# Performance work log

Measured on AMD Instinct MI355X. Metric: run time of the kernel, lower is better.

The kernel has to match this reference:

```python
import jax, jax.numpy as jnp
import numpy as np

N1, N2, F = 512, 512, 128
H = 512  # hidden width


def _xavier(key, shape):
    fan_in, fan_out = shape
    std = (2.0 / (fan_in + fan_out)) ** 0.5
    return jax.random.normal(key, shape, dtype=jnp.float32) * std


def setup_inputs() -> dict:
    key = jax.random.key(0)
    ks = jax.random.split(key, 8)
    V1 = jax.random.normal(ks[0], (1, N1, F), dtype=jnp.float32)
    V2 = jax.random.normal(ks[1], (1, N2, F), dtype=jnp.float32)
    W1 = _xavier(ks[2], (2 * F, H))
    b1 = 0.0001 + 5e-05 * jax.random.normal(ks[3], (H,), dtype=jnp.float32)
    W2 = _xavier(ks[4], (H, H))
    b2 = 0.0001 + 5e-05 * jax.random.normal(ks[5], (H,), dtype=jnp.float32)
    W3 = _xavier(ks[6], (H, 2))
    b3 = 0.0001 + 5e-05 * jax.random.normal(ks[7], (2,), dtype=jnp.float32)
    return {"V1": V1, "V2": V2, "W1": W1, "b1": b1, "W2": W2, "b2": b2, "W3": W3, "b3": b3}


def reference(V1, V2, W1, b1, W2, b2, W3, b3):
    n1, n2, f = V1.shape[1], V2.shape[1], V1.shape[2]
    # Fused broadcast-concat replacing the N1*N2 Python double loop
    # (i outer, j inner; V1[i] first, V2[j] second -> row-major reshape matches stack order)
    pairs = jnp.concatenate([
        jnp.broadcast_to(V1[0][:, None, :], (n1, n2, f)),
        jnp.broadcast_to(V2[0][None, :, :], (n1, n2, f)),
    ], axis=-1).reshape(1, n1 * n2, 2 * f)
    h = jax.nn.relu(pairs @ W1 + b1)
    h = jax.nn.relu(h @ W2 + b2)
    out = jax.nn.relu(h @ W3 + b3)  # final LinearEmbedding also has ReLU by default
    return out
```

## Files before the change

### kernel.cpp

```cpp
#include <hip/hip_runtime.h>


typedef short bf16x8 __attribute__((ext_vector_type(8)));
typedef float f32x16 __attribute__((ext_vector_type(16)));

#define NROW 512
#define FDIM 128
#define HDIM 512

__device__ __forceinline__ unsigned int pk2(float x, float y) {
  unsigned int r;
  asm("v_cvt_pk_bf16_f32 %0, %1, %2" : "=v"(r) : "v"(x), "v"(y));
  return r;
}

__global__ __launch_bounds__(256) void prep_ab(
    const float* __restrict__ V1, const float* __restrict__ V2,
    const float* __restrict__ W1, const float* __restrict__ b1,
    float* __restrict__ Ap, float* __restrict__ Bp) {
  __shared__ float sv[4 * FDIM];
  const int b = blockIdx.x;
  const int t = threadIdx.x;
  const bool isB = b >= 128;
  const int r0 = (b & 127) * 4;
  const float* V = isB ? V2 : V1;
  const float* W = W1 + (isB ? FDIM * HDIM : 0);
  for (int idx = t; idx < 4 * FDIM; idx += 256) sv[idx] = V[r0 * FDIM + idx];
  __syncthreads();
  float s[4][2] = {};
  for (int k = 0; k < FDIM; ++k) {
    const float w0 = W[k * HDIM + t];
    const float w1 = W[k * HDIM + t + 256];
#pragma unroll
    for (int r = 0; r < 4; ++r) {
      const float v = sv[r * FDIM + k];
      s[r][0] += v * w0;
      s[r][1] += v * w1;
    }
  }
  float* O = isB ? Bp : Ap;
  const float bb0 = isB ? 0.f : b1[t];
  const float bb1 = isB ? 0.f : b1[t + 256];
#pragma unroll
  for (int r = 0; r < 4; ++r) {
    O[(r0 + r) * HDIM + t] = s[r][0] + bb0;
    O[(r0 + r) * HDIM + t + 256] = s[r][1] + bb1;
  }
}

__global__ __launch_bounds__(256) void prep_w2(const float* __restrict__ W2,
                                               unsigned short* __restrict__ W2T) {
  const int o = blockIdx.x * 256 + threadIdx.x;
  const int kc = o >> 9;
  const int n = o & 511;
  unsigned int u[4];
#pragma unroll
  for (int e2 = 0; e2 < 4; ++e2)
    u[e2] = pk2(W2[(kc * 8 + 2 * e2) * HDIM + n], W2[(kc * 8 + 2 * e2 + 1) * HDIM + n]);
  *(uint4*)(W2T + (size_t)o * 8) = make_uint4(u[0], u[1], u[2], u[3]);
}

__global__ __launch_bounds__(512, 2) void mlp_main(
    const float* __restrict__ Ap, const float* __restrict__ Bp,
    const unsigned short* __restrict__ W2T, const float* __restrict__ b2,
    const float* __restrict__ W3, const float* __restrict__ b3,
    float* __restrict__ out) {
  extern __shared__ char smem[];
  char* sA = smem;

  const int tid = threadIdx.x;
  const int wave = tid >> 6;
  const int lane = tid & 63;
  const int cl = lane & 31;
  const int hi = lane >> 5;
  const int r15 = lane & 15;

  const int m0 = blockIdx.x * 128;
  const int i = m0 >> 9;
  const int j0 = m0 & 511;

  {
    const int c = tid & 63;
    const int rsub = tid >> 6;
    const float4 a0 = *(const float4*)(Ap + i * HDIM + c * 8);
    const float4 a1 = *(const float4*)(Ap + i * HDIM + c * 8 + 4);
#pragma unroll
    for (int it = 0; it < 16; ++it) {
      const int row = it * 8 + rsub;
      const float4 g0 = *(const float4*)(Bp + (size_t)(j0 + row) * HDIM + c * 8);
      const float4 g1 = *(const float4*)(Bp + (size_t)(j0 + row) * HDIM + c * 8 + 4);
      const uint4 v = make_uint4(
          pk2(fmaxf(a0.x + g0.x, 0.f), fmaxf(a0.y + g0.y, 0.f)),
          pk2(fmaxf(a0.z + g0.z, 0.f), fmaxf(a0.w + g0.w, 0.f)),
          pk2(fmaxf(a1.x + g1.x, 0.f), fmaxf(a1.y + g1.y, 0.f)),
          pk2(fmaxf(a1.z + g1.z, 0.f), fmaxf(a1.w + g1.w, 0.f)));
      *(uint4*)(sA + row * 1024 + ((c ^ (row & 15)) << 4)) = v;
    }
  }

  float w30[2], w31[2], bb[2];
#pragma unroll
  for (int nt = 0; nt < 2; ++nt) {
    const int n = (wave << 6) + (nt << 5) + cl;
    w30[nt] = W3[2 * n];
    w31[nt] = W3[2 * n + 1];
    bb[nt] = b2[n];
  }
  const float bb3_0 = b3[0], bb3_1 = b3[1];

  __syncthreads();

  f32x16 acc[4][2];
#pragma unroll
  for (int mt = 0; mt < 4; ++mt)
#pragma unroll
    for (int nt = 0; nt < 2; ++nt)
#pragma unroll
      for (int q = 0; q < 16; ++q) acc[mt][nt][q] = 0.f;

  const char* abase0 = sA + cl * 1024;
  const char* bbase = (const char*)W2T + (((wave << 6) + cl) << 4) + (hi << 13);

  bf16x8 af[2][4], bfr[3][2];
  {
    const int off = (hi ^ r15) << 4;
#pragma unroll
    for (int mt = 0; mt < 4; ++mt) af[0][mt] = *(const bf16x8*)(abase0 + mt * 32768 + off);
#pragma unroll
    for (int q = 0; q < 3; ++q) {
      const char* bp = bbase + ((size_t)q << 14);
      bfr[q][0] = *(const bf16x8*)(bp);
      bfr[q][1] = *(const bf16x8*)(bp + (1 << 9));
    }
  }
#pragma unroll
  for (int s = 0; s < 32; ++s) {
    const int cur = s & 1;
    if (s < 31) {
      const int off = ((((s + 1) << 1) | hi) ^ r15) << 4;
#pragma unroll
      for (int mt = 0; mt < 4; ++mt)
        af[cur ^ 1][mt] = *(const bf16x8*)(abase0 + mt * 32768 + off);
    }
    if (s < 30) {
      const char* bp = bbase + ((size_t)(s + 2) << 14);
      bfr[(s + 2) % 3][0] = *(const bf16x8*)(bp);
      bfr[(s + 2) % 3][1] = *(const bf16x8*)(bp + (1 << 9));
    }
    __builtin_amdgcn_s_setprio(1);
#pragma unroll
    for (int nt = 0; nt < 2; ++nt)
#pragma unroll
      for (int mt = 0; mt < 4; ++mt)
        acc[mt][nt] = __builtin_amdgcn_mfma_f32_32x32x16_bf16(af[cur][mt], bfr[s % 3][nt],
                                                              acc[mt][nt], 0, 0, 0);
    __builtin_amdgcn_s_setprio(0);
  }

  __syncthreads();

#pragma unroll
  for (int mt = 0; mt < 4; ++mt) {
#pragma unroll
    for (int rp = 0; rp < 8; ++rp) {
      const int ra = 2 * rp;
      const float h0a = fmaxf(acc[mt][0][ra] + bb[0], 0.f);
      const float h1a = fmaxf(acc[mt][1][ra] + bb[1], 0.f);
      const float h0b = fmaxf(acc[mt][0][ra + 1] + bb[0], 0.f);
      const float h1b = fmaxf(acc[mt][1][ra + 1] + bb[1], 0.f);
      const float4 v = make_float4(h0a * w30[0] + h1a * w30[1], h0a * w31[0] + h1a * w31[1],
                                   h0b * w30[0] + h1b * w30[1], h0b * w31[0] + h1b * w31[1]);
      const int rpi = ((ra & 3) + 8 * (ra >> 2) + 4 * hi) >> 1;
      *(float4*)(smem + rpi * 4096 + (((wave << 5) + cl) << 4)) = v;
    }
    __syncthreads();
    if (tid < 256) {
      const int rpi = tid >> 4;
      const int sub = tid & 15;
      float4 s = make_float4(0.f, 0.f, 0.f, 0.f);
#pragma unroll
      for (int k = 0; k < 16; ++k) {
        const float4 v = *(const float4*)(smem + rpi * 4096 + ((sub + (k << 4)) << 4));
        s.x += v.x; s.y += v.y; s.z += v.z; s.w += v.w;
      }
#pragma unroll
      for (int d = 1; d < 16; d <<= 1) {
        s.x += __shfl_xor(s.x, d, 64);
        s.y += __shfl_xor(s.y, d, 64);
        s.z += __shfl_xor(s.z, d, 64);
        s.w += __shfl_xor(s.w, d, 64);
      }
      if (sub == 0) {
        const int rg = m0 + (mt << 5) + (rpi << 1);
        *(float4*)(out + rg * 2) =
            make_float4(fmaxf(s.x + bb3_0, 0.f), fmaxf(s.y + bb3_1, 0.f),
                        fmaxf(s.z + bb3_0, 0.f), fmaxf(s.w + bb3_1, 0.f));
      }
    }
    __syncthreads();
  }
}

extern "C" void kernel_launch(void* const* d_in, const int* in_sizes, int n_in,
                              void* d_out, int out_size, void* d_ws, size_t ws_size,
                              hipStream_t stream) {
  const float* V1 = (const float*)d_in[0];
  const float* V2 = (const float*)d_in[1];
  const float* W1 = (const float*)d_in[2];
  const float* b1 = (const float*)d_in[3];
  const float* W2 = (const float*)d_in[4];
  const float* b2 = (const float*)d_in[5];
  const float* W3 = (const float*)d_in[6];
  const float* b3 = (const float*)d_in[7];

  float* Ap = (float*)d_ws;
  float* Bp = Ap + NROW * HDIM;
  unsigned short* W2T = (unsigned short*)(Bp + NROW * HDIM);

  const int smem_bytes = 131072;
  (void)hipFuncSetAttribute((const void*)mlp_main,
                            hipFuncAttributeMaxDynamicSharedMemorySize, smem_bytes);

  prep_ab<<<256, 256, 0, stream>>>(V1, V2, W1, b1, Ap, Bp);
  prep_w2<<<128, 256, 0, stream>>>(W2, W2T);
  mlp_main<<<2048, 512, smem_bytes, stream>>>(Ap, Bp, W2T, b2, W3, b3, (float*)d_out);
}
```

Measured before the change: 152.5 us.

## Make main kernel persistent and overlap A-tile construction with MFMA via K-half double buffering

The main kernel now launches 256 blocks, each looping over 8 row tiles, instead of one block per tile. The bf16 A tile is split into two K-halves held in double-buffered LDS. Each half for the next stage (the second half of this tile, or the first half of the next tile) is built from Ap/Bp and written while MFMAs run on the current half. This hides the global-load and convert cost of the A fill that previously ran serially before compute, and W2 fragments are prefetched across tile boundaries. In exchange, LDS grows to 160KB, the epilogue is split into smaller reduction rounds with more barriers, s_setprio hints are dropped, and the last tile prefetches one row past Ap.

```diff
diff --git a/kernel.cpp b/kernel.cpp
--- a/kernel.cpp
+++ b/kernel.cpp
@@ -60,13 +60,28 @@
   *(uint4*)(W2T + (size_t)o * 8) = make_uint4(u[0], u[1], u[2], u[3]);
 }
 
+__device__ __forceinline__ void fill_w(char* sAbuf, int w, int rsub, int c32,
+                                       const float4& a0, const float4& a1,
+                                       const float* bpn) {
+  const int row = w * 16 + rsub;
+  const float* bp = bpn + (size_t)row * HDIM;
+  const float4 g0 = *(const float4*)(bp);
+  const float4 g1 = *(const float4*)(bp + 4);
+  const uint4 v = make_uint4(
+      pk2(fmaxf(a0.x + g0.x, 0.f), fmaxf(a0.y + g0.y, 0.f)),
+      pk2(fmaxf(a0.z + g0.z, 0.f), fmaxf(a0.w + g0.w, 0.f)),
+      pk2(fmaxf(a1.x + g1.x, 0.f), fmaxf(a1.y + g1.y, 0.f)),
+      pk2(fmaxf(a1.z + g1.z, 0.f), fmaxf(a1.w + g1.w, 0.f)));
+  *(uint4*)(sAbuf + row * 512 + ((c32 ^ rsub) << 4)) = v;
+}
+
 __global__ __launch_bounds__(512, 2) void mlp_main(
     const float* __restrict__ Ap, const float* __restrict__ Bp,
     const unsigned short* __restrict__ W2T, const float* __restrict__ b2,
     const float* __restrict__ W3, const float* __restrict__ b3,
     float* __restrict__ out) {
   extern __shared__ char smem[];
-  char* sA = smem;
+  char* epi = smem + 131072;
 
   const int tid = threadIdx.x;
   const int wave = tid >> 6;
@@ -74,29 +89,9 @@
   const int cl = lane & 31;
   const int hi = lane >> 5;
   const int r15 = lane & 15;
-
-  const int m0 = blockIdx.x * 128;
-  const int i = m0 >> 9;
-  const int j0 = m0 & 511;
-
-  {
-    const int c = tid & 63;
-    const int rsub = tid >> 6;
-    const float4 a0 = *(const float4*)(Ap + i * HDIM + c * 8);
-    const float4 a1 = *(const float4*)(Ap + i * HDIM + c * 8 + 4);
-#pragma unroll
-    for (int it = 0; it < 16; ++it) {
-      const int row = it * 8 + rsub;
-      const float4 g0 = *(const float4*)(Bp + (size_t)(j0 + row) * HDIM + c * 8);
-      const float4 g1 = *(const float4*)(Bp + (size_t)(j0 + row) * HDIM + c * 8 + 4);
-      const uint4 v = make_uint4(
-          pk2(fmaxf(a0.x + g0.x, 0.f), fmaxf(a0.y + g0.y, 0.f)),
-          pk2(fmaxf(a0.z + g0.z, 0.f), fmaxf(a0.w + g0.w, 0.f)),
-          pk2(fmaxf(a1.x + g1.x, 0.f), fmaxf(a1.y + g1.y, 0.f)),
-          pk2(fmaxf(a1.z + g1.z, 0.f), fmaxf(a1.w + g1.w, 0.f)));
-      *(uint4*)(sA + row * 1024 + ((c ^ (row & 15)) << 4)) = v;
-    }
-  }
+  const int c32 = tid & 31;
+  const int rsub = tid >> 5;
+  const int bid = blockIdx.x;
 
   float w30[2], w31[2], bb[2];
 #pragma unroll
@@ -108,96 +103,136 @@
   }
   const float bb3_0 = b3[0], bb3_1 = b3[1];
 
+  const char* bbase = (const char*)W2T + (((wave << 6) + cl) << 4) + (hi << 13);
+
+  f32x16 acc[4][2];
+#pragma unroll
+  for (int mt = 0; mt < 4; ++mt)
+#pragma unroll
+    for (int nt = 0; nt < 2; ++nt)
+#pragma unroll
+      for (int q = 0; q < 16; ++q) acc[mt][nt][q] = 0.f;
+
+  bf16x8 af[2][4], bfr[4][2];
+
+#pragma unroll
+  for (int q = 0; q < 3; ++q) {
+    const char* bp = bbase + ((size_t)q << 14);
+    bfr[q][0] = *(const bf16x8*)(bp);
+    bfr[q][1] = *(const bf16x8*)(bp + (1 << 9));
+  }
+
+  {
+    const int m00 = bid * 1024;
+    const int i0 = m00 >> 9;
+    const int j00 = m00 & 511;
+    const int kh = c32 * 8;
+    const float4 a0 = *(const float4*)(Ap + i0 * HDIM + kh);
+    const float4 a1 = *(const float4*)(Ap + i0 * HDIM + kh + 4);
+    const float* bpn = Bp + (size_t)j00 * HDIM + kh;
+#pragma unroll
+    for (int w = 0; w < 8; ++w) fill_w(smem, w, rsub, c32, a0, a1, bpn);
+  }
   __syncthreads();
 
-  f32x16 acc[4][2];
-#pragma unroll
-  for (int mt = 0; mt < 4; ++mt)
-#pragma unroll
-    for (int nt = 0; nt < 2; ++nt)
-#pragma unroll
-      for (int q = 0; q < 16; ++q) acc[mt][nt][q] = 0.f;
-
-  const char* abase0 = sA + cl * 1024;
-  const char* bbase = (const char*)W2T + (((wave << 6) + cl) << 4) + (hi << 13);
-
-  bf16x8 af[2][4], bfr[3][2];
-  {
-    const int off = (hi ^ r15) << 4;
-#pragma unroll
-    for (int mt = 0; mt < 4; ++mt) af[0][mt] = *(const bf16x8*)(abase0 + mt * 32768 + off);
-#pragma unroll
-    for (int q = 0; q < 3; ++q) {
-      const char* bp = bbase + ((size_t)q << 14);
-      bfr[q][0] = *(const bf16x8*)(bp);
-      bfr[q][1] = *(const bf16x8*)(bp + (1 << 9));
+  for (int t = 0; t < 8; ++t) {
+    const int tl = bid * 8 + t;
+    const int m0 = tl * 128;
+#pragma unroll
+    for (int h = 0; h < 2; ++h) {
+      char* sAbuf = smem + h * 65536;
+      char* sAnext = smem + (h ^ 1) * 65536;
+      const int tln = (h == 0) ? tl : tl + 1;
+      const int hn = h ^ 1;
+      const int m0n = tln * 128;
+      const int in_ = m0n >> 9;
+      const int j0n = m0n & 511;
+      const int khn = hn * 256 + c32 * 8;
+      const float4 a0n = *(const float4*)(Ap + (size_t)in_ * HDIM + khn);
+      const float4 a1n = *(const float4*)(Ap + (size_t)in_ * HDIM + khn + 4);
+      const float* bpn = Bp + (size_t)j0n * HDIM + khn;
+
+      const char* alane = sAbuf + cl * 512;
+      {
+        const int off = (hi ^ r15) << 4;
+#pragma unroll
+        for (int mt = 0; mt < 4; ++mt)
+          af[0][mt] = *(const bf16x8*)(alane + mt * 16384 + off);
+      }
+#pragma unroll
+      for (int s = 0; s < 16; ++s) {
+        const int sg = h * 16 + s;
+        {
+          const int pg = (sg + 3) & 31;
+          const char* bp = bbase + ((size_t)pg << 14);
+          bfr[pg & 3][0] = *(const bf16x8*)(bp);
+          bfr[pg & 3][1] = *(const bf16x8*)(bp + (1 << 9));
+        }
+        if (s < 15) {
+          const int off = ((((s + 1) << 1) | hi) ^ r15) << 4;
+#pragma unroll
+          for (int mt = 0; mt < 4; ++mt)
+            af[(s + 1) & 1][mt] = *(const bf16x8*)(alane + mt * 16384 + off);
+        }
+        if (s & 1) fill_w(sAnext, s >> 1, rsub, c32, a0n, a1n, bpn);
+#pragma unroll
+        for (int nt = 0; nt < 2; ++nt)
+#pragma unroll
+          for (int mt = 0; mt < 4; ++mt)
+            acc[mt][nt] = __builtin_amdgcn_mfma_f32_32x32x16_bf16(
+                af[s & 1][mt], bfr[sg & 3][nt], acc[mt][nt], 0, 0, 0);
+      }
+      __syncthreads();
     }
-  }
-#pragma unroll
-  for (int s = 0; s < 32; ++s) {
-    const int cur = s & 1;
-    if (s < 31) {
-      const int off = ((((s + 1) << 1) | hi) ^ r15) << 4;
-#pragma unroll
-      for (int mt = 0; mt < 4; ++mt)
-        af[cur ^ 1][mt] = *(const bf16x8*)(abase0 + mt * 32768 + off);
+
+#pragma unroll
+    for (int mt = 0; mt < 4; ++mt) {
+#pragma unroll
+      for (int g = 0; g < 2; ++g) {
+#pragma unroll
+        for (int rr = 0; rr < 4; ++rr) {
+          const int ra = 8 * g + 2 * rr;
+          const float h0a = fmaxf(acc[mt][0][ra] + bb[0], 0.f);
+          const float h1a = fmaxf(acc[mt][1][ra] + bb[1], 0.f);
+          const float h0b = fmaxf(acc[mt][0][ra + 1] + bb[0], 0.f);
+          const float h1b = fmaxf(acc[mt][1][ra + 1] + bb[1], 0.f);
+          const float4 v =
+              make_float4(h0a * w30[0] + h1a * w30[1], h0a * w31[0] + h1a * w31[1],
+                          h0b * w30[0] + h1b * w30[1], h0b * w31[0] + h1b * w31[1]);
+          const int rpi_l = (((ra & 7) & 3) + 8 * ((ra & 7) >> 2) + 4 * hi) >> 1;
+          *(float4*)(epi + rpi_l * 4096 + (((wave << 5) + cl) << 4)) = v;
+        }
+        __syncthreads();
+        if (tid < 128) {
+          const int rpi_l = tid >> 4;
+          const int sub = tid & 15;
+          float4 s = make_float4(0.f, 0.f, 0.f, 0.f);
+#pragma unroll
+          for (int k = 0; k < 16; ++k) {
+            const float4 v = *(const float4*)(epi + rpi_l * 4096 + ((sub + (k << 4)) << 4));
+            s.x += v.x; s.y += v.y; s.z += v.z; s.w += v.w;
+          }
+#pragma unroll
+          for (int d = 1; d < 16; d <<= 1) {
+            s.x += __shfl_xor(s.x, d, 64);
+            s.y += __shfl_xor(s.y, d, 64);
+            s.z += __shfl_xor(s.z, d, 64);
+            s.w += __shfl_xor(s.w, d, 64);
+          }
+          if (sub == 0) {
+            const int rg = m0 + (mt << 5) + (g << 4) + (rpi_l << 1);
+            *(float4*)(out + rg * 2) =
+                make_float4(fmaxf(s.x + bb3_0, 0.f), fmaxf(s.y + bb3_1, 0.f),
+                            fmaxf(s.z + bb3_0, 0.f), fmaxf(s.w + bb3_1, 0.f));
+          }
+        }
+        __syncthreads();
+      }
+#pragma unroll
+      for (int nt = 0; nt < 2; ++nt)
+#pragma unroll
+        for (int q = 0; q < 16; ++q) acc[mt][nt][q] = 0.f;
     }
-    if (s < 30) {
-      const char* bp = bbase + ((size_t)(s + 2) << 14);
-      bfr[(s + 2) % 3][0] = *(const bf16x8*)(bp);
-      bfr[(s + 2) % 3][1] = *(const bf16x8*)(bp + (1 << 9));
-    }
-    __builtin_amdgcn_s_setprio(1);
-#pragma unroll
-    for (int nt = 0; nt < 2; ++nt)
-#pragma unroll
-      for (int mt = 0; mt < 4; ++mt)
-        acc[mt][nt] = __builtin_amdgcn_mfma_f32_32x32x16_bf16(af[cur][mt], bfr[s % 3][nt],
-                                                              acc[mt][nt], 0, 0, 0);
-    __builtin_amdgcn_s_setprio(0);
-  }
-
-  __syncthreads();
-
-#pragma unroll
-  for (int mt = 0; mt < 4; ++mt) {
-#pragma unroll
-    for (int rp = 0; rp < 8; ++rp) {
-      const int ra = 2 * rp;
-      const float h0a = fmaxf(acc[mt][0][ra] + bb[0], 0.f);
-      const float h1a = fmaxf(acc[mt][1][ra] + bb[1], 0.f);
-      const float h0b = fmaxf(acc[mt][0][ra + 1] + bb[0], 0.f);
-      const float h1b = fmaxf(acc[mt][1][ra + 1] + bb[1], 0.f);
-      const float4 v = make_float4(h0a * w30[0] + h1a * w30[1], h0a * w31[0] + h1a * w31[1],
-                                   h0b * w30[0] + h1b * w30[1], h0b * w31[0] + h1b * w31[1]);
-      const int rpi = ((ra & 3) + 8 * (ra >> 2) + 4 * hi) >> 1;
-      *(float4*)(smem + rpi * 4096 + (((wave << 5) + cl) << 4)) = v;
-    }
-    __syncthreads();
-    if (tid < 256) {
-      const int rpi = tid >> 4;
-      const int sub = tid & 15;
-      float4 s = make_float4(0.f, 0.f, 0.f, 0.f);
-#pragma unroll
-      for (int k = 0; k < 16; ++k) {
-        const float4 v = *(const float4*)(smem + rpi * 4096 + ((sub + (k << 4)) << 4));
-        s.x += v.x; s.y += v.y; s.z += v.z; s.w += v.w;
-      }
-#pragma unroll
-      for (int d = 1; d < 16; d <<= 1) {
-        s.x += __shfl_xor(s.x, d, 64);
-        s.y += __shfl_xor(s.y, d, 64);
-        s.z += __shfl_xor(s.z, d, 64);
-        s.w += __shfl_xor(s.w, d, 64);
-      }
-      if (sub == 0) {
-        const int rg = m0 + (mt << 5) + (rpi << 1);
-        *(float4*)(out + rg * 2) =
-            make_float4(fmaxf(s.x + bb3_0, 0.f), fmaxf(s.y + bb3_1, 0.f),
-                        fmaxf(s.z + bb3_0, 0.f), fmaxf(s.w + bb3_1, 0.f));
-      }
-    }
-    __syncthreads();
   }
 }
 
@@ -217,11 +252,11 @@
   float* Bp = Ap + NROW * HDIM;
   unsigned short* W2T = (unsigned short*)(Bp + NROW * HDIM);
 
-  const int smem_bytes = 131072;
+  const int smem_bytes = 163840;
   (void)hipFuncSetAttribute((const void*)mlp_main,
                             hipFuncAttributeMaxDynamicSharedMemorySize, smem_bytes);
 
   prep_ab<<<256, 256, 0, stream>>>(V1, V2, W1, b1, Ap, Bp);
   prep_w2<<<128, 256, 0, stream>>>(W2, W2T);
-  mlp_main<<<2048, 512, smem_bytes, stream>>>(Ap, Bp, W2T, b2, W3, b3, (float*)d_out);
-}
+  mlp_main<<<256, 512, smem_bytes, stream>>>(Ap, Bp, W2T, b2, W3, b3, (float*)d_out);
+}
```

After: 389.9 us. 156% more time.

## Deepen W2 register prefetch, hoist it before A staging, and halve epilogue barriers

Applied to the files above, without the earlier changes.

The W2 fragment register ring grows from 3 to 5 stages, so B loads are issued 4 steps ahead. The first four stages, along with the W3/b2/b3 loads, are now issued before the shared-memory A tile is built, so their global latency overlaps that staging work. The epilogue handles two m-tiles per round in separate 64KB shared buffers, with all 512 threads reducing instead of 256. This halves the number of barrier pairs, at the cost of more live vector registers, which could cause spills or lower occupancy under the 512x2 launch bound.

```diff
diff --git a/kernel.cpp b/kernel.cpp
--- a/kernel.cpp
+++ b/kernel.cpp
@@ -79,6 +79,25 @@
   const int i = m0 >> 9;
   const int j0 = m0 & 511;
 
+  const char* bbase = (const char*)W2T + (((wave << 6) + cl) << 4) + (hi << 13);
+
+  bf16x8 af[2][4], bfr[5][2];
+#pragma unroll
+  for (int q = 0; q < 4; ++q) {
+    const char* bp = bbase + ((size_t)q << 14);
+    bfr[q][0] = *(const bf16x8*)(bp);
+    bfr[q][1] = *(const bf16x8*)(bp + (1 << 9));
+  }
+  float w30[2], w31[2], bb[2];
+#pragma unroll
+  for (int nt = 0; nt < 2; ++nt) {
+    const int n = (wave << 6) + (nt << 5) + cl;
+    w30[nt] = W3[2 * n];
+    w31[nt] = W3[2 * n + 1];
+    bb[nt] = b2[n];
+  }
+  const float bb3_0 = b3[0], bb3_1 = b3[1];
+
   {
     const int c = tid & 63;
     const int rsub = tid >> 6;
@@ -97,17 +116,6 @@
       *(uint4*)(sA + row * 1024 + ((c ^ (row & 15)) << 4)) = v;
     }
   }
-
-  float w30[2], w31[2], bb[2];
-#pragma unroll
-  for (int nt = 0; nt < 2; ++nt) {
-    const int n = (wave << 6) + (nt << 5) + cl;
-    w30[nt] = W3[2 * n];
-    w31[nt] = W3[2 * n + 1];
-    bb[nt] = b2[n];
-  }
-  const float bb3_0 = b3[0], bb3_1 = b3[1];
-
   __syncthreads();
 
   f32x16 acc[4][2];
@@ -119,19 +127,10 @@
       for (int q = 0; q < 16; ++q) acc[mt][nt][q] = 0.f;
 
   const char* abase0 = sA + cl * 1024;
-  const char* bbase = (const char*)W2T + (((wave << 6) + cl) << 4) + (hi << 13);
-
-  bf16x8 af[2][4], bfr[3][2];
   {
     const int off = (hi ^ r15) << 4;
 #pragma unroll
     for (int mt = 0; mt < 4; ++mt) af[0][mt] = *(const bf16x8*)(abase0 + mt * 32768 + off);
-#pragma unroll
-    for (int q = 0; q < 3; ++q) {
-      const char* bp = bbase + ((size_t)q << 14);
-      bfr[q][0] = *(const bf16x8*)(bp);
-      bfr[q][1] = *(const bf16x8*)(bp + (1 << 9));
-    }
   }
 #pragma unroll
   for (int s = 0; s < 32; ++s) {
@@ -142,17 +141,17 @@
       for (int mt = 0; mt < 4; ++mt)
         af[cur ^ 1][mt] = *(const bf16x8*)(abase0 + mt * 32768 + off);
     }
-    if (s < 30) {
-      const char* bp = bbase + ((size_t)(s + 2) << 14);
-      bfr[(s + 2) % 3][0] = *(const bf16x8*)(bp);
-      bfr[(s + 2) % 3][1] = *(const bf16x8*)(bp + (1 << 9));
+    if (s < 28) {
+      const char* bp = bbase + ((size_t)(s + 4) << 14);
+      bfr[(s + 4) % 5][0] = *(const bf16x8*)(bp);
+      bfr[(s + 4) % 5][1] = *(const bf16x8*)(bp + (1 << 9));
     }
     __builtin_amdgcn_s_setprio(1);
 #pragma unroll
     for (int nt = 0; nt < 2; ++nt)
 #pragma unroll
       for (int mt = 0; mt < 4; ++mt)
-        acc[mt][nt] = __builtin_amdgcn_mfma_f32_32x32x16_bf16(af[cur][mt], bfr[s % 3][nt],
+        acc[mt][nt] = __builtin_amdgcn_mfma_f32_32x32x16_bf16(af[cur][mt], bfr[s % 5][nt],
                                                               acc[mt][nt], 0, 0, 0);
     __builtin_amdgcn_s_setprio(0);
   }
@@ -160,41 +159,50 @@
   __syncthreads();
 
 #pragma unroll
-  for (int mt = 0; mt < 4; ++mt) {
-#pragma unroll
-    for (int rp = 0; rp < 8; ++rp) {
-      const int ra = 2 * rp;
-      const float h0a = fmaxf(acc[mt][0][ra] + bb[0], 0.f);
-      const float h1a = fmaxf(acc[mt][1][ra] + bb[1], 0.f);
-      const float h0b = fmaxf(acc[mt][0][ra + 1] + bb[0], 0.f);
-      const float h1b = fmaxf(acc[mt][1][ra + 1] + bb[1], 0.f);
-      const float4 v = make_float4(h0a * w30[0] + h1a * w30[1], h0a * w31[0] + h1a * w31[1],
-                                   h0b * w30[0] + h1b * w30[1], h0b * w31[0] + h1b * w31[1]);
-      const int rpi = ((ra & 3) + 8 * (ra >> 2) + 4 * hi) >> 1;
-      *(float4*)(smem + rpi * 4096 + (((wave << 5) + cl) << 4)) = v;
+  for (int rnd = 0; rnd < 2; ++rnd) {
+#pragma unroll
+    for (int ml = 0; ml < 2; ++ml) {
+      const int mt = rnd * 2 + ml;
+      char* ebuf = smem + ml * 65536;
+#pragma unroll
+      for (int rp = 0; rp < 8; ++rp) {
+        const int ra = 2 * rp;
+        const float h0a = fmaxf(acc[mt][0][ra] + bb[0], 0.f);
+        const float h1a = fmaxf(acc[mt][1][ra] + bb[1], 0.f);
+        const float h0b = fmaxf(acc[mt][0][ra + 1] + bb[0], 0.f);
+        const float h1b = fmaxf(acc[mt][1][ra + 1] + bb[1], 0.f);
+        const float4 v =
+            make_float4(h0a * w30[0] + h1a * w30[1], h0a * w31[0] + h1a * w31[1],
+                        h0b * w30[0] + h1b * w30[1], h0b * w31[0] + h1b * w31[1]);
+        const int rpi = ((ra & 3) + 8 * (ra >> 2) + 4 * hi) >> 1;
+        *(float4*)(ebuf + rpi * 4096 + (((wave << 5) + cl) << 4)) = v;
+      }
     }
     __syncthreads();
-    if (tid < 256) {
-      const int rpi = tid >> 4;
-      const int sub = tid & 15;
-      float4 s = make_float4(0.f, 0.f, 0.f, 0.f);
+    {
+      const int ml = tid >> 8;
+      const int t2 = tid & 255;
+      const int rpi = t2 >> 4;
+      const int sub = t2 & 15;
+      const char* ebuf = smem + ml * 65536;
+      float4 s4 = make_float4(0.f, 0.f, 0.f, 0.f);
 #pragma unroll
       for (int k = 0; k < 16; ++k) {
-        const float4 v = *(const float4*)(smem + rpi * 4096 + ((sub + (k << 4)) << 4));
-        s.x += v.x; s.y += v.y; s.z += v.z; s.w += v.w;
+        const float4 v = *(const float4*)(ebuf + rpi * 4096 + ((sub + (k << 4)) << 4));
+        s4.x += v.x; s4.y += v.y; s4.z += v.z; s4.w += v.w;
       }
 #pragma unroll
       for (int d = 1; d < 16; d <<= 1) {
-        s.x += __shfl_xor(s.x, d, 64);
-        s.y += __shfl_xor(s.y, d, 64);
-        s.z += __shfl_xor(s.z, d, 64);
-        s.w += __shfl_xor(s.w, d, 64);
+        s4.x += __shfl_xor(s4.x, d, 64);
+        s4.y += __shfl_xor(s4.y, d, 64);
+        s4.z += __shfl_xor(s4.z, d, 64);
+        s4.w += __shfl_xor(s4.w, d, 64);
       }
       if (sub == 0) {
-        const int rg = m0 + (mt << 5) + (rpi << 1);
+        const int rg = m0 + ((rnd * 2 + ml) << 5) + (rpi << 1);
         *(float4*)(out + rg * 2) =
-            make_float4(fmaxf(s.x + bb3_0, 0.f), fmaxf(s.y + bb3_1, 0.f),
-                        fmaxf(s.z + bb3_0, 0.f), fmaxf(s.w + bb3_1, 0.f));
+            make_float4(fmaxf(s4.x + bb3_0, 0.f), fmaxf(s4.y + bb3_1, 0.f),
+                        fmaxf(s4.z + bb3_0, 0.f), fmaxf(s4.w + bb3_1, 0.f));
       }
     }
     __syncthreads();
```

Result: faster. 149.1 us (-2.2%).
